# Kernel optimization log

Measured on AMD Instinct MI355X. Metric: run time of the kernel, lower is better.

The kernel has to match this reference:

```python
import jax, jax.numpy as jnp
import numpy as np

B, T, F = 32, 1024, 64
H = 128          # num_lstm_out
KH = 16          # kan_hidden_dim
C1, C2, C3 = 128, 256, 128
NC = 10


def _glorot(key, shape):
    fan_in = shape[0] if len(shape) == 2 else int(np.prod(shape[1:]))
    return (jax.random.normal(key, shape, jnp.float32) / np.sqrt(fan_in)).astype(jnp.float32)


def setup_inputs() -> dict:
    key = jax.random.key(0)
    ks = jax.random.split(key, 24)
    D = F + H
    d = {}
    d['x'] = jax.random.normal(ks[0], (B, T, F), jnp.float32)
    d['eps_z'] = jax.random.normal(ks[1], (B, H), jnp.float32)
    d['eps_cat'] = jax.random.normal(ks[2], (B, H), jnp.float32)
    # KAN-LSTM cell: gates = W2 @ silu(W1 @ [x;h])
    d['kan_w1'] = _glorot(ks[3], (D, KH)); d['kan_b1'] = jnp.zeros((KH,), jnp.float32)
    d['kan_w2'] = _glorot(ks[4], (KH, 4 * H)); d['kan_b2'] = jnp.zeros((4 * H,), jnp.float32)
    # causal convs (OIH layout)
    d['conv1_w'] = _glorot(ks[5], (C1, F, 8)); d['conv1_b'] = jnp.zeros((C1,), jnp.float32)
    d['conv2_w'] = _glorot(ks[6], (C2, C1, 5)); d['conv2_b'] = jnp.zeros((C2,), jnp.float32)
    d['conv3_w'] = _glorot(ks[7], (C3, C2, 3)); d['conv3_b'] = jnp.zeros((C3,), jnp.float32)
    # batchnorm affine params
    d['bn1_g'] = jnp.ones((C1,), jnp.float32); d['bn1_b'] = jnp.zeros((C1,), jnp.float32)
    d['bn2_g'] = jnp.ones((C2,), jnp.float32); d['bn2_b'] = jnp.zeros((C2,), jnp.float32)
    d['bn3_g'] = jnp.ones((C3,), jnp.float32); d['bn3_b'] = jnp.zeros((C3,), jnp.float32)
    # SE layers (reduction=16, no bias)
    d['se1_w1'] = _glorot(ks[8], (C1, C1 // 16)); d['se1_w2'] = _glorot(ks[9], (C1 // 16, C1))
    d['se2_w1'] = _glorot(ks[10], (C2, C2 // 16)); d['se2_w2'] = _glorot(ks[11], (C2 // 16, C2))
    # VIB heads
    d['fc_mu_w'] = _glorot(ks[12], (H, H)); d['fc_mu_b'] = jnp.zeros((H,), jnp.float32)
    d['fc_std_w'] = _glorot(ks[13], (H, H)); d['fc_std_b'] = jnp.zeros((H,), jnp.float32)
    d['fc_mu_cat_w'] = _glorot(ks[14], (2 * H, H)); d['fc_mu_cat_b'] = jnp.zeros((H,), jnp.float32)
    d['fc_std_cat_w'] = _glorot(ks[15], (2 * H, H)); d['fc_std_cat_b'] = jnp.zeros((H,), jnp.float32)
    d['fc_w'] = _glorot(ks[16], (H + C3, NC)); d['fc_b'] = jnp.zeros((NC,), jnp.float32)
    return d


def _kan_lstm(x, w1, b1, w2, b2):
    # x: (B,T,F) -> hidden (B,T,H); sequential recurrence via lax.scan
    xT = jnp.swapaxes(x, 0, 1)  # (T,B,F)
    h0 = jnp.zeros((x.shape[0], H), x.dtype)
    c0 = jnp.zeros((x.shape[0], H), x.dtype)

    def step(carry, xt):
        h, c = carry
        g = jax.nn.silu(jnp.concatenate([xt, h], axis=-1) @ w1 + b1) @ w2 + b2  # (B,4H)
        i_, f_, g_, o_ = jnp.split(g, 4, axis=-1)
        c = jax.nn.sigmoid(f_) * c + jax.nn.sigmoid(i_) * jnp.tanh(g_)
        h = jax.nn.sigmoid(o_) * jnp.tanh(c)
        return (h, c), h

    _, hs = jax.lax.scan(step, (h0, c0), xT)
    return jnp.swapaxes(hs, 0, 1)  # (B,T,H)


def _cluster_hidden(hidden):
    # hidden: (B,T,H). Pairwise cosine sim -> exp kernel -> best 2-block cut.
    Tn = hidden.shape[1]
    last = hidden[:, -1, :]
    hn = hidden / jnp.clip(jnp.linalg.norm(hidden, axis=-1, keepdims=True), 1e-8)
    S = jnp.exp(-5.5 * (1.0 - jnp.einsum('bik,bjk->bij', hn, hn)))  # (B,T,T)
    S = S * (1.0 - jnp.eye(Tn, dtype=S.dtype))  # zero diagonal
    # 2D prefix sums give all block sums in O(T^2) instead of O(T^3)
    P = jnp.cumsum(jnp.cumsum(S, axis=1), axis=2)
    i = jnp.arange(1, Tn)
    TL = P[:, i - 1, i - 1]                 # (B,T-1) sum of [:i,:i]
    full = P[:, -1, -1][:, None]
    TR = P[:, i - 1, -1] - TL               # sum of [:i,i:]
    BL = P[:, -1, i - 1] - TL               # sum of [i:,:i]
    BR = full - TL - TR - BL                # sum of [i:,i:]
    ii = i.astype(S.dtype)
    nn = (Tn - i).astype(S.dtype)
    dist = TL / (ii * ii) + BR / (nn * nn) - (TR + BL) / (ii * nn)
    cuts = jnp.argmax(dist, axis=1) + 1     # (B,)
    mask = (jnp.arange(Tn)[None, :] < cuts[:, None]).astype(hidden.dtype)
    corr = jnp.einsum('bt,bth->bh', mask, hidden) / cuts[:, None].astype(hidden.dtype)
    return last, corr


def _causal_conv(x, w, b):
    k = w.shape[-1]
    xp = jnp.pad(x, ((0, 0), (0, 0), (k - 1, 0)))
    y = jax.lax.conv_general_dilated(xp, w, (1,), 'VALID',
                                     dimension_numbers=('NCH', 'OIH', 'NCH'))
    return y + b[None, :, None]


def _bn(x, g, b, eps=1e-3):
    m = x.mean(axis=(0, 2), keepdims=True)
    v = x.var(axis=(0, 2), keepdims=True)
    return (x - m) / jnp.sqrt(v + eps) * g[None, :, None] + b[None, :, None]


def _se(x, w1, w2):
    y = x.mean(axis=2)                       # (B,C)
    y = jax.nn.sigmoid(jax.nn.relu(y @ w1) @ w2)
    return x * y[:, :, None]


def reference(x, eps_z, eps_cat, kan_w1, kan_b1, kan_w2, kan_b2,
              conv1_w, conv1_b, conv2_w, conv2_b, conv3_w, conv3_b,
              bn1_g, bn1_b, bn2_g, bn2_b, bn3_g, bn3_b,
              se1_w1, se1_w2, se2_w1, se2_w2,
              fc_mu_w, fc_mu_b, fc_std_w, fc_std_b,
              fc_mu_cat_w, fc_mu_cat_b, fc_std_cat_w, fc_std_cat_b,
              fc_w, fc_b):
    # LSTM branch
    hidden = _kan_lstm(x, kan_w1, kan_b1, kan_w2, kan_b2)      # (B,T,H)
    out, corr = _cluster_hidden(hidden)
    mu = corr @ fc_mu_w + fc_mu_b
    std = jax.nn.softplus(corr @ fc_std_w + fc_std_b)
    z = mu + std * eps_z
    xz = jnp.concatenate([out, z], axis=1)                      # (B,2H)
    mu_cat = xz @ fc_mu_cat_w + fc_mu_cat_b
    std_cat = jax.nn.softplus(xz @ fc_std_cat_w + fc_std_cat_b)
    x1 = mu_cat + std_cat * eps_cat   # dropout in eval mode = identity
    # FCN branch
    x2 = jnp.swapaxes(x, 1, 2)                                  # (B,F,T)
    x2 = jax.nn.gelu(_bn(_causal_conv(x2, conv1_w, conv1_b), bn1_g, bn1_b), approximate=False)
    x2 = _se(x2, se1_w1, se1_w2)
    x2 = jax.nn.gelu(_bn(_causal_conv(x2, conv2_w, conv2_b), bn2_g, bn2_b), approximate=False)
    x2 = _se(x2, se2_w1, se2_w2)
    x2 = jax.nn.gelu(_bn(_causal_conv(x2, conv3_w, conv3_b), bn3_g, bn3_b), approximate=False)
    x2 = x2.mean(axis=2)                                        # (B,C3)
    x_all = jnp.concatenate([x1, x2], axis=1)
    logits = x_all @ fc_w + fc_b
    return (jax.nn.log_softmax(logits, axis=1), mu, std, mu_cat, std_cat)
```

## Files before the change

kernel.cpp:

```cpp
#include <hip/hip_runtime.h>
#include <math.h>

#define B_ 32
#define T_ 1024
#define F_ 64
#define H_ 128
#define D_ 192
#define KH_ 16
#define C1_ 128
#define C2_ 256
#define C3_ 128
#define NC_ 10

typedef float v2f __attribute__((ext_vector_type(2)));
typedef float f32x4 __attribute__((ext_vector_type(4)));
typedef __bf16 bfrag __attribute__((ext_vector_type(8)));

__device__ __forceinline__ float sig_(float x){ return 1.f/(1.f+__expf(-x)); }
__device__ __forceinline__ float tanh_(float x){ return 1.f - 2.f/(__expf(2.f*x)+1.f); }
__device__ __forceinline__ float gelu_(float x){ return 0.5f*x*(1.f+erff(x*0.70710678118654752f)); }
__device__ __forceinline__ float softplus_(float x){ return fmaxf(x,0.f) + log1pf(__expf(-fabsf(x))); }

__device__ __forceinline__ unsigned bfpack(float a, float b){
  unsigned ua = __float_as_uint(a), ub = __float_as_uint(b);
  ua = ua + 0x7FFFu + ((ua>>16)&1u);
  ub = ub + 0x7FFFu + ((ub>>16)&1u);
  return (ua>>16) | (ub & 0xFFFF0000u);
}
__device__ __forceinline__ unsigned short bf1(float a){
  unsigned ua = __float_as_uint(a);
  ua = ua + 0x7FFFu + ((ua>>16)&1u);
  return (unsigned short)(ua>>16);
}
__device__ __forceinline__ float bf2f(unsigned short h){
  return __uint_as_float(((unsigned)h)<<16);
}

#define QPERM_XOR1(x) __int_as_float(__builtin_amdgcn_mov_dpp(__float_as_int(x), 0xB1, 0xF, 0xF, true))
#define QPERM_XOR2(x) __int_as_float(__builtin_amdgcn_mov_dpp(__float_as_int(x), 0x4E, 0xF, 0xF, true))

#define LDS_BARRIER() asm volatile("s_waitcnt lgkmcnt(0)\n\ts_barrier" ::: "memory")


__device__ __forceinline__ void ax_body(int blk, char* smemraw,
    const float* __restrict__ x, const float* __restrict__ w1, const float* __restrict__ b1,
    float* __restrict__ axT)
{
  struct AxS { float xs[16][68]; float w1s[64][16]; };
  AxS* sm = (AxS*)smemraw;
  const int bt0 = blk*16;
  const int tid = threadIdx.x;
  for(int i=tid;i<64*16;i+=256){ sm->w1s[i>>4][i&15] = w1[i]; }
  for(int i=tid;i<16*64;i+=256){ const int r=i>>6, d=i&63; sm->xs[r][d] = x[(size_t)(bt0+r)*64 + d]; }
  __syncthreads();
  const int r = tid>>4, j = tid&15;
  float s = b1[j];
  #pragma unroll
  for(int d=0; d<64; d++) s += sm->xs[r][d]*sm->w1s[d][j];
  const int bt = bt0 + r;
  axT[((size_t)(bt>>10)*16 + j)*1024 + (bt&1023)] = s;
}

__device__ __forceinline__ void prepack_body(int blk,
    const float* __restrict__ w1s, const float* __restrict__ w2s, const float* __restrict__ w3s,
    unsigned short* __restrict__ wp1, unsigned short* __restrict__ wp2, unsigned short* __restrict__ wp3)
{
  int e = blk*256 + threadIdx.x;
  if(e >= 65536+163840+98304) return;
  const float* w; unsigned short* wp; int Cout, Cin, Kw;
  if(e < 65536){ w=w1s; wp=wp1; Cout=C1_; Cin=F_;  Kw=8; }
  else if(e < 65536+163840){ e-=65536; w=w2s; wp=wp2; Cout=C2_; Cin=C1_; Kw=5; }
  else { e-=229376; w=w3s; wp=wp3; Cout=C3_; Cin=C2_; Kw=3; }
  const int co = e/(Cin*Kw);
  const int rem = e - co*(Cin*Kw);
  const int ci = rem/Kw, kw = rem - ci*Kw;
  const int off = (((ci>>5)*Kw + kw)*(Cout>>4) + (co>>4))*512 + ((co&15)*4 + ((ci>>3)&3))*8 + (ci&7);
  wp[off] = bf1(w[e]);
}

__device__ __forceinline__ void norm8_body(size_t rowbase,
    const float* __restrict__ hidden,
    unsigned short* __restrict__ hnhi, unsigned short* __restrict__ hnlo)
{
  const size_t row = rowbase + (threadIdx.x>>5);
  const int l = threadIdx.x&31;
  const float* hr = hidden + row*H_;
  float s = 0.f;
  for(int k=l;k<H_;k+=32){ float v=hr[k]; s+=v*v; }
  #pragma unroll
  for(int m=16;m>=1;m>>=1) s += __shfl_xor(s, m, 64);
  const float inv = 1.f/fmaxf(sqrtf(s), 1e-8f);
  const float4 v = *(const float4*)&hr[l*4];
  const float f0=v.x*inv, f1=v.y*inv, f2=v.z*inv, f3=v.w*inv;
  const unsigned short h0=bf1(f0), h1=bf1(f1), h2=bf1(f2), h3=bf1(f3);
  uint2 phi; phi.x = (unsigned)h0 | ((unsigned)h1<<16); phi.y = (unsigned)h2 | ((unsigned)h3<<16);
  *(uint2*)&hnhi[row*H_ + l*4] = phi;
  const unsigned short g0=bf1(f0-bf2f(h0)), g1=bf1(f1-bf2f(h1)), g2=bf1(f2-bf2f(h2)), g3=bf1(f3-bf2f(h3));
  uint2 plo; plo.x = (unsigned)g0 | ((unsigned)g1<<16); plo.y = (unsigned)g2 | ((unsigned)g3<<16);
  *(uint2*)&hnlo[row*H_ + l*4] = plo;
}

__device__ __forceinline__ void chunk_body(int b, int c, char* smemraw,
    const float* __restrict__ hidden, float* __restrict__ chunksum)
{
  float* red = (float*)smemraw;
  const int tid = threadIdx.x, h = tid&127, half = tid>>7;
  const float* hb = hidden + ((size_t)b*T_ + c*64)*H_;
  float s = 0.f;
  for(int t=half; t<64; t+=2) s += hb[(size_t)t*H_ + h];
  if(half==1) red[h] = s;
  __syncthreads();
  if(half==0) chunksum[((size_t)b*16 + c)*H_ + h] = s + red[h];
}

struct SS {
  unsigned short Ahi[64*136];
  unsigned short Alo[64*136];
  unsigned short Bhi[64*136];
  unsigned short Blo[64*136];
  double red[64][17];
};
__device__ __forceinline__ void s_list_body(int b, int f0, int cnt, char* smemraw,
    const unsigned short* __restrict__ hnhi, const unsigned short* __restrict__ hnlo,
    double* __restrict__ rowsum, double* __restrict__ psum)
{
  SS* sm = (SS*)smemraw;
  const int tid = threadIdx.x, l = tid & 63, wv = tid >> 6;
  const int m = l & 15, q = l >> 4;
  const int arow = (wv*16 + m)*136;
  double* red = &sm->red[0][0];
  int curj = -1;

  for(int f=f0; f<f0+cnt; f++){
    int j = (int)((sqrtf(8.f*(float)f + 1.f) - 1.f)*0.5f);
    while((j*(j+1))/2 > f) j--;
    while(((j+1)*(j+2))/2 <= f) j++;
    const int i = f - (j*(j+1))/2;
    const int i0 = i*64, j0 = j*64;

    __syncthreads();
    if(j != curj){
      curj = j;
      const uint4* ghi = (const uint4*)(hnhi + ((size_t)b*T_ + j0)*H_);
      const uint4* glo = (const uint4*)(hnlo + ((size_t)b*T_ + j0)*H_);
      for(int t2=tid; t2<64*16; t2+=256){
        const int r = t2>>4, c8 = t2&15;
        *(uint4*)&sm->Bhi[r*136 + c8*8] = ghi[r*16 + c8];
        *(uint4*)&sm->Blo[r*136 + c8*8] = glo[r*16 + c8];
      }
    }
    {
      const uint4* ghi = (const uint4*)(hnhi + ((size_t)b*T_ + i0)*H_);
      const uint4* glo = (const uint4*)(hnlo + ((size_t)b*T_ + i0)*H_);
      for(int t2=tid; t2<64*16; t2+=256){
        const int r = t2>>4, c8 = t2&15;
        *(uint4*)&sm->Ahi[r*136 + c8*8] = ghi[r*16 + c8];
        *(uint4*)&sm->Alo[r*136 + c8*8] = glo[r*16 + c8];
      }
    }
    __syncthreads();

    f32x4 acc[4];
    #pragma unroll
    for(int nt=0;nt<4;nt++) acc[nt] = (f32x4)(0.f);
    #pragma unroll
    for(int kc=0;kc<4;kc++){
      const bfrag Ah = *(const bfrag*)&sm->Ahi[arow + kc*32 + q*8];
      const bfrag Al = *(const bfrag*)&sm->Alo[arow + kc*32 + q*8];
      #pragma unroll
      for(int nt=0;nt<4;nt++){
        const int brow = (nt*16 + m)*136 + kc*32 + q*8;
        const bfrag Bh = *(const bfrag*)&sm->Bhi[brow];
        const bfrag Bl = *(const bfrag*)&sm->Blo[brow];
        acc[nt] = __builtin_amdgcn_mfma_f32_16x16x32_bf16(Ah, Bh, acc[nt], 0, 0, 0);
        acc[nt] = __builtin_amdgcn_mfma_f32_16x16x32_bf16(Al, Bh, acc[nt], 0, 0, 0);
        acc[nt] = __builtin_amdgcn_mfma_f32_16x16x32_bf16(Ah, Bl, acc[nt], 0, 0, 0);
      }
    }

    if(i0 == j0){
      double rs[4]={0,0,0,0}, ps[4]={0,0,0,0};
      #pragma unroll
      for(int nt=0;nt<4;nt++){
        const int gj = j0 + nt*16 + m;
        #pragma unroll
        for(int r=0;r<4;r++){
          const int gi = i0 + wv*16 + q*4 + r;
          if(gi == gj) continue;
          const float sv = __expf(-5.5f*(1.f - acc[nt][r]));
          rs[r] += (double)sv;
          if(gj < gi) ps[r] += (double)sv;
        }
      }
      #pragma unroll
      for(int r=0;r<4;r++){
        #pragma unroll
        for(int mk=1;mk<16;mk<<=1){
          rs[r] += __shfl_xor(rs[r], mk, 64);
          ps[r] += __shfl_xor(ps[r], mk, 64);
        }
      }
      if(m == 0){
        const size_t gbase = (size_t)b*T_ + i0 + wv*16 + q*4;
        #pragma unroll
        for(int r=0;r<4;r++){
          unsafeAtomicAdd(&rowsum[gbase + r], rs[r]);
          unsafeAtomicAdd(&psum[gbase + r], ps[r]);
        }
      }
    } else {
      double rs[4]={0,0,0,0}, cs[4]={0,0,0,0};
      #pragma unroll
      for(int nt=0;nt<4;nt++){
        double csn = 0.0;
        #pragma unroll
        for(int r=0;r<4;r++){
          const float sv = __expf(-5.5f*(1.f - acc[nt][r]));
          rs[r] += (double)sv;
          csn   += (double)sv;
        }
        cs[nt] = csn;
      }
      #pragma unroll
      for(int r=0;r<4;r++){
        #pragma unroll
        for(int mk=1;mk<16;mk<<=1) rs[r] += __shfl_xor(rs[r], mk, 64);
      }
      if(m == 0){
        const size_t gbase = (size_t)b*T_ + i0 + wv*16 + q*4;
        #pragma unroll
        for(int r=0;r<4;r++) unsafeAtomicAdd(&rowsum[gbase + r], rs[r]);
      }
      #pragma unroll
      for(int nt=0;nt<4;nt++){
        cs[nt] += __shfl_xor(cs[nt], 16, 64);
        cs[nt] += __shfl_xor(cs[nt], 32, 64);
      }
      if(q == 0){
        #pragma unroll
        for(int nt=0;nt<4;nt++) red[wv*64 + nt*16 + m] = cs[nt];
      }
      __syncthreads();
      if(tid < 64){
        const double v = red[tid] + red[64+tid] + red[128+tid] + red[192+tid];
        unsafeAtomicAdd(&rowsum[(size_t)b*T_ + j0 + tid], v);
        unsafeAtomicAdd(&psum[(size_t)b*T_ + j0 + tid], v);
      }
    }
  }
}

struct CS {
  double sr[256]; double sp[256]; double bd[256]; double totR;
  float c2[2][128]; int bidx[256]; int cut;
};
__device__ __forceinline__ void cluster_body(int b, char* smemraw,
    const double* __restrict__ rowsum, const double* __restrict__ psum,
    const float* __restrict__ hidden, const float* __restrict__ chunksum,
    float* __restrict__ corr, int* __restrict__ cuts)
{
  CS* sm = (CS*)smemraw;
  const int tid = threadIdx.x;
  const double* r = rowsum + (size_t)b*T_;
  const double* p = psum + (size_t)b*T_;
  double r4[4], p4[4];
  #pragma unroll
  for(int q=0;q<4;q++){ r4[q]=r[tid*4+q]; p4[q]=p[tid*4+q]; }
  sm->sr[tid]=r4[0]+r4[1]+r4[2]+r4[3];
  sm->sp[tid]=p4[0]+p4[1]+p4[2]+p4[3];
  __syncthreads();
  if(tid==0){
    double ar=0, ap=0;
    for(int i=0;i<256;i++){ double tr=sm->sr[i], tp=sm->sp[i]; sm->sr[i]=ar; sm->sp[i]=ap; ar+=tr; ap+=tp; }
    sm->totR = ar;
  }
  __syncthreads();
  double cr = sm->sr[tid], cp = sm->sp[tid];
  const double full = sm->totR;
  double best = -1e308; int bi = 1;
  #pragma unroll
  for(int q=0;q<4;q++){
    cr += r4[q]; cp += p4[q];
    const int i = 4*tid + q + 1;
    if(i < T_){
      const double TL = 2.0*cp;
      const double TRv = cr - TL;
      const double BR = full - TL - 2.0*TRv;
      const double di = (double)i, dn = (double)(T_-i);
      const double dist = TL/(di*di) + BR/(dn*dn) - (2.0*TRv)/(di*dn);
      if(dist > best){ best=dist; bi=i; }
    }
  }
  sm->bd[tid]=best; sm->bidx[tid]=bi;
  __syncthreads();
  if(tid==0){
    double bb=-1e308; int ii=1;
    for(int q=0;q<256;q++){ if(sm->bd[q]>bb){ bb=sm->bd[q]; ii=sm->bidx[q]; } }
    sm->cut=ii; cuts[b]=ii;
  }
  __syncthreads();
  const int cut = sm->cut;
  const int h = tid&127, half = tid>>7;
  float s=0.f;
  if(half==0){
    const int cf = cut>>6;
    for(int c=0;c<cf;c++) s += chunksum[((size_t)b*16 + c)*H_ + h];
  } else {
    const float* hb = hidden + (size_t)b*T_*H_;
    for(int t=(cut & ~63); t<cut; t++) s += hb[(size_t)t*H_ + h];
  }
  sm->c2[half][h]=s;
  __syncthreads();
  if(tid<128) corr[b*H_+tid] = (sm->c2[0][tid]+sm->c2[1][tid])/(float)cut;
}

__device__ __forceinline__ void head1_body(int b, char* smemraw,
    const float* __restrict__ corr, const float* __restrict__ hidden,
    const float* __restrict__ eps_z, const float* __restrict__ eps_cat,
    const float* __restrict__ mu_w, const float* __restrict__ mu_b,
    const float* __restrict__ std_w, const float* __restrict__ std_b,
    const float* __restrict__ muc_w, const float* __restrict__ muc_b,
    const float* __restrict__ stdc_w, const float* __restrict__ stdc_b,
    float* __restrict__ out_mu, float* __restrict__ out_std,
    float* __restrict__ out_muc, float* __restrict__ out_stdc, float* __restrict__ x1)
{
  struct H1 { float cs[128]; float xz[256]; };
  H1* sm = (H1*)smemraw;
  const int h = threadIdx.x;
  if(h<128){
    sm->cs[h]=corr[b*H_+h];
    sm->xz[h]=hidden[((size_t)b*T_ + (T_-1))*H_ + h];
  }
  __syncthreads();
  if(h<128){
    float m=mu_b[h], sdv=std_b[h];
    for(int k=0;k<H_;k++){ const float cv=sm->cs[k]; m+=cv*mu_w[k*H_+h]; sdv+=cv*std_w[k*H_+h]; }
    const float stdv = softplus_(sdv);
    out_mu[b*H_+h]=m; out_std[b*H_+h]=stdv;
    sm->xz[128+h] = m + stdv*eps_z[b*H_+h];
  }
  __syncthreads();
  if(h<128){
    float mc=muc_b[h], sc=stdc_b[h];
    for(int k=0;k<256;k++){ const float v=sm->xz[k]; mc+=v*muc_w[k*H_+h]; sc+=v*stdc_w[k*H_+h]; }
    const float stdc = softplus_(sc);
    out_muc[b*H_+h]=mc; out_stdc[b*H_+h]=stdc;
    x1[b*H_+h]=mc + stdc*eps_cat[b*H_+h];
  }
}

struct ConvS {
  float sescale[256];
  float seh[16];
  unsigned short xs[72*40];
};
__device__ __forceinline__ void conv_body(int bx, int by, int bz, char* smemraw,
    const float* __restrict__ in, const unsigned short* __restrict__ wp,
    const float* __restrict__ bias,
    const float* __restrict__ se_in, const float* __restrict__ se_w1,
    const float* __restrict__ se_w2, int seR,
    float* __restrict__ y, float* __restrict__ bnacc, int Cin, int Cout, int Kw)
{
  ConvS* sm = (ConvS*)smemraw;
  unsigned short* xs = sm->xs;
  const int b = bz, t0 = bx*64, co0 = by*64;
  const int tid = threadIdx.x, l = tid&63, wv = tid>>6;
  const int q = l>>4, m = l&15;
  const int TW = 64 + Kw - 1;
  const int abase = (wv*16 + m)*40 + q*8;
  const int boff = (m*4 + q)*8;
  const bool use_se = (se_in != nullptr);

  if(use_se){
    float* ms = (float*)xs;
    if(tid<Cin) ms[tid] = se_in[b*Cin+tid] * (1.f/(float)T_);
    __syncthreads();
    if(tid<seR){ float s=0.f; for(int k=0;k<Cin;k++) s += ms[k]*se_w1[k*seR+tid]; sm->seh[tid]=fmaxf(s,0.f); }
    __syncthreads();
    if(tid<Cin){ float s=0.f; for(int k=0;k<seR;k++) s += sm->seh[k]*se_w2[k*Cin+tid]; sm->sescale[tid]=sig_(s); }
  }

  f32x4 acc[4];
  #pragma unroll
  for(int nt=0;nt<4;nt++) acc[nt] = (f32x4)(0.f);

  const int nchunks = Cin >> 5;
  for(int cc=0; cc<nchunks; cc++){
    __syncthreads();
    for(int idx=tid; idx<TW*8; idx+=256){
      const int r = idx>>3, c4 = (idx&7)*4;
      const int tg = t0 - (Kw-1) + r;
      uint2 pk = make_uint2(0u, 0u);
      if(tg >= 0){
        float4 v = *(const float4*)&in[((size_t)b*T_ + tg)*Cin + cc*32 + c4];
        if(use_se){
          const float4 s4 = *(const float4*)&sm->sescale[cc*32 + c4];
          v.x*=s4.x; v.y*=s4.y; v.z*=s4.z; v.w*=s4.w;
        }
        pk.x = bfpack(v.x, v.y); pk.y = bfpack(v.z, v.w);
      }
      *(uint2*)&xs[r*40 + c4] = pk;
    }
    __syncthreads();
    for(int kw=0; kw<Kw; kw++){
      const bfrag Af = *(const bfrag*)&xs[abase + kw*40];
      #pragma unroll
      for(int nt=0; nt<4; nt++){
        const unsigned short* wpp = wp + ((size_t)((cc*Kw + kw)*(Cout>>4) + (by*4 + nt)))*512 + boff;
        const bfrag Bf = *(const bfrag*)wpp;
        acc[nt] = __builtin_amdgcn_mfma_f32_16x16x32_bf16(Af, Bf, acc[nt], 0, 0, 0);
      }
    }
  }
  __syncthreads();
  float* part = (float*)xs;
  const int t_base = t0 + wv*16 + q*4;
  #pragma unroll
  for(int nt=0; nt<4; nt++){
    const int co = co0 + nt*16 + m;
    const float bv = bias[co];
    float s1 = 0.f, s2 = 0.f;
    #pragma unroll
    for(int r=0;r<4;r++){
      const float v = acc[nt][r] + bv;
      y[((size_t)b*T_ + t_base + r)*Cout + co] = v;
      s1 += v; s2 += v*v;
    }
    s1 += __shfl_xor(s1, 16); s1 += __shfl_xor(s1, 32);
    s2 += __shfl_xor(s2, 16); s2 += __shfl_xor(s2, 32);
    if(q==0){ part[(wv*64 + nt*16 + m)*2+0] = s1; part[(wv*64 + nt*16 + m)*2+1] = s2; }
  }
  __syncthreads();
  if(tid < 64){
    float a1=0.f, a2=0.f;
    #pragma unroll
    for(int w2i=0; w2i<4; w2i++){ a1 += part[(w2i*64+tid)*2+0]; a2 += part[(w2i*64+tid)*2+1]; }
    atomicAdd(&bnacc[co0 + tid], a1);
    atomicAdd(&bnacc[Cout + co0 + tid], a2);
  }
}

__device__ __forceinline__ void bn_act_body(int b, int chunk, char* smemraw,
    float* __restrict__ y, const float* __restrict__ bnacc,
    const float* __restrict__ gw, const float* __restrict__ bw,
    float* __restrict__ mean_acc, int C, int write_y)
{
  const int t0 = chunk*128, tid = threadIdx.x;
  const int c = tid & (C-1), part = tid / C, np = 256 / C;
  const float cnt = (float)(B_*T_);
  const float mm = bnacc[c]/cnt;
  const float var = bnacc[C+c]/cnt - mm*mm;
  const float sc = gw[c]/sqrtf(var+1e-3f);
  const float sh = bw[c] - mm*sc;
  float s = 0.f;
  for(int t=t0+part; t<t0+128; t+=np){
    const size_t off = ((size_t)b*T_ + t)*C + c;
    float v = y[off];
    v = gelu_(v*sc + sh);
    if(write_y) y[off] = v;
    s += v;
  }
  float* rs = (float*)smemraw;
  if(np > 1){
    rs[tid]=s;
    __syncthreads();
    if(part==0) s += rs[tid+C];
  }
  if(part==0) atomicAdd(&mean_acc[b*C+c], s);
}

__device__ __forceinline__ void lstm_seg_body(int b, int ts, int nsteps, char* smemraw,
    const float* __restrict__ axT, const float* __restrict__ w1,
    const float* __restrict__ w2, const float* __restrict__ b2,
    float* __restrict__ hidden, float* __restrict__ cstate)
{
  float (*hs)[148] = (float(*)[148])smemraw;
  const int tid = threadIdx.x;
  const int l = tid & 63, wv = tid >> 6;
  const int j = l >> 2, g = l & 3;
  const int hi = wv*64 + l;

  v2f w1hv[16];
  #pragma unroll
  for(int q=0;q<16;q++){
    w1hv[q].x = w1[(64 + g*32 + 2*q)*KH_ + j];
    w1hv[q].y = w1[(64 + g*32 + 2*q + 1)*KH_ + j];
  }
  v2f w2if[16], w2go[16];
  #pragma unroll
  for(int k=0;k<16;k++){
    w2if[k].x = w2[k*512 + hi];       w2if[k].y = w2[k*512 + 128 + hi];
    w2go[k].x = w2[k*512 + 256 + hi]; w2go[k].y = w2[k*512 + 384 + hi];
  }
  v2f bif, bgo;
  bif.x = b2[hi]; bif.y = b2[128+hi]; bgo.x = b2[256+hi]; bgo.y = b2[384+hi];

  const float* axr = axT + ((size_t)b*16 + j)*1024;
  float* hb = hidden + (size_t)b*T_*H_;
  const int hwi = (hi>>5)*36 + (hi&31);
  float c;
  if(ts == 0){
    for(int i=tid;i<2*148;i+=128) ((float*)hs)[i]=0.f;
    c = 0.f;
  } else {
    c = cstate[b*H_ + hi];
    hs[0][hwi] = hb[(size_t)(ts-1)*H_ + hi];
  }
  float4 axA = *(const float4*)&axr[ts];
  float4 axB = *(const float4*)&axr[ts+4];
  __syncthreads();

#define LSTM_STEP(tt, axv, RB) { \
    const float* hsr = hs[RB]; \
    float* hsw = hs[1-(RB)]; \
    v2f ap0=(v2f)(0.f), ap1=(v2f)(0.f), ap2=(v2f)(0.f), ap3=(v2f)(0.f); \
    { const float4 hv = *(const float4*)&hsr[g*36 + 0];  ap0 += ((v2f){hv.x,hv.y})*w1hv[0]  + ((v2f){hv.z,hv.w})*w1hv[1]; } \
    { const float4 hv = *(const float4*)&hsr[g*36 + 4];  ap1 += ((v2f){hv.x,hv.y})*w1hv[2]  + ((v2f){hv.z,hv.w})*w1hv[3]; } \
    { const float4 hv = *(const float4*)&hsr[g*36 + 8];  ap2 += ((v2f){hv.x,hv.y})*w1hv[4]  + ((v2f){hv.z,hv.w})*w1hv[5]; } \
    { const float4 hv = *(const float4*)&hsr[g*36 + 12]; ap3 += ((v2f){hv.x,hv.y})*w1hv[6]  + ((v2f){hv.z,hv.w})*w1hv[7]; } \
    { const float4 hv = *(const float4*)&hsr[g*36 + 16]; ap0 += ((v2f){hv.x,hv.y})*w1hv[8]  + ((v2f){hv.z,hv.w})*w1hv[9]; } \
    { const float4 hv = *(const float4*)&hsr[g*36 + 20]; ap1 += ((v2f){hv.x,hv.y})*w1hv[10] + ((v2f){hv.z,hv.w})*w1hv[11]; } \
    { const float4 hv = *(const float4*)&hsr[g*36 + 24]; ap2 += ((v2f){hv.x,hv.y})*w1hv[12] + ((v2f){hv.z,hv.w})*w1hv[13]; } \
    { const float4 hv = *(const float4*)&hsr[g*36 + 28]; ap3 += ((v2f){hv.x,hv.y})*w1hv[14] + ((v2f){hv.z,hv.w})*w1hv[15]; } \
    const v2f apt = (ap0+ap1)+(ap2+ap3); \
    float a = apt.x + apt.y; \
    a += QPERM_XOR1(a); \
    a += QPERM_XOR2(a); \
    a += (axv); \
    const float g1 = a * sig_(a); \
    v2f aIF = bif, aGO = bgo; \
    _Pragma("unroll") \
    for(int k=0;k<16;k++){ \
      const float gk = __int_as_float(__builtin_amdgcn_readlane(__float_as_int(g1), 4*k)); \
      v2f gk2; gk2.x=gk; gk2.y=gk; \
      aIF += gk2 * w2if[k]; \
      aGO += gk2 * w2go[k]; \
    } \
    const float si = sig_(aIF.x); \
    const float sf = sig_(aIF.y); \
    const float tg = tanh_(aGO.x); \
    const float so = sig_(aGO.y); \
    c = sf*c + si*tg; \
    const float h = so * tanh_(c); \
    hsw[hwi] = h; \
    hb[(size_t)(tt)*H_ + hi] = h; \
    LDS_BARRIER(); \
  }

  const int te = ts + nsteps;
  for(int t0=ts;t0<te;t0+=4){
    const int tl = (t0+8 < 1020) ? (t0+8) : 1020;
    const float4 axC = *(const float4*)&axr[tl];
    LSTM_STEP(t0+0, axA.x, 0)
    LSTM_STEP(t0+1, axA.y, 1)
    LSTM_STEP(t0+2, axA.z, 0)
    LSTM_STEP(t0+3, axA.w, 1)
    axA = axB; axB = axC;
  }
#undef LSTM_STEP
  if(te < T_) cstate[b*H_ + hi] = c;
}


__global__ __launch_bounds__(256) void mega0_kernel(
    const float* c1w, const float* c2w, const float* c3w,
    unsigned short* wp1, unsigned short* wp2, unsigned short* wp3,
    const float* x, const float* kw1, const float* kb1, float* axT)
{
  __shared__ __align__(16) char sm[16*68*4 + 64*16*4];
  const int bid = blockIdx.x;
  if(bid < 256) prepack_body(bid, c1w, c2w, c3w, wp1, wp2, wp3);
  else ax_body(bid-256, sm, x, kw1, kb1, axT);
}

__global__ __launch_bounds__(256) void seg_kernel(
    int ts, int nsteps, int phase, int nphase, int nxtra,
    int nr0, int nnorm, int c0, int nchunk,
    const float* axT, const float* kw1, const float* kw2, const float* kb2,
    float* hidden, float* cstate,
    const float* x, const unsigned short* wp1, const float* c1b, float* y1, float* bn1,
    const float* g1w, const float* b1w, float* se1_in,
    const unsigned short* wp2, const float* c2b, const float* s1w1, const float* s1w2,
    float* y2, float* bn2,
    const float* g2w, const float* b2w, float* se2_in,
    const unsigned short* wp3, const float* c3b, const float* s2w1, const float* s2w2,
    float* y3, float* bn3,
    const float* c1w, const float* c2w, const float* c3w,
    unsigned short* wp1o, unsigned short* wp2o, unsigned short* wp3o,
    unsigned short* hnhi, unsigned short* hnlo, float* chunksum)
{
  __shared__ __align__(16) char sm[sizeof(ConvS)];
  const int bid = blockIdx.x;
  if(bid < 32){
    if(nsteps == 0) return;
    if(threadIdx.x >= 128){
      const int nb = nsteps + 1;
      #pragma nounroll
      for(int i=0;i<nb;i++){ asm volatile("s_barrier" ::: "memory"); }
      return;
    }
    __builtin_amdgcn_s_setprio(1);
    lstm_seg_body(bid, ts, nsteps, sm, axT, kw1, kw2, kb2, hidden, cstate);
    return;
  }
  int cb = bid - 32;
  if(cb < nphase){
    switch(phase){
      case 0:
        conv_body(cb&15, (cb>>4)&1, cb>>5, sm, x, wp1, c1b,
                  nullptr, nullptr, nullptr, 0, y1, bn1, F_, C1_, 8);
        break;
      case 1:
        bn_act_body(cb>>3, cb&7, sm, y1, bn1, g1w, b1w, se1_in, C1_, 1);
        break;
      case 2:
        conv_body(cb&15, (cb>>4)&3, cb>>6, sm, y1, wp2, c2b,
                  se1_in, s1w1, s1w2, C1_/16, y2, bn2, C1_, C2_, 5);
        break;
      case 3:
        bn_act_body(cb>>3, cb&7, sm, y2, bn2, g2w, b2w, se2_in, C2_, 1);
        break;
      default:
        conv_body(cb&15, (cb>>4)&1, cb>>5, sm, y2, wp3, c3b,
                  se2_in, s2w1, s2w2, C2_/16, y3, bn3, C2_, C3_, 3);
        break;
    }
    return;
  }
  cb -= nphase;
  if(cb < nxtra){ prepack_body(256 + cb, c1w, c2w, c3w, wp1o, wp2o, wp3o); return; }
  cb -= nxtra;
  if(cb < nnorm){
    const int b = cb & 31, tb = cb >> 5;
    norm8_body((size_t)b*T_ + nr0 + tb*8, hidden, hnhi, hnlo);
    return;
  }
  cb -= nnorm;
  if(cb < nchunk){
    const int b = cb & 31;
    chunk_body(b, c0 + (cb>>5), sm, hidden, chunksum);
  }
}

__global__ __launch_bounds__(256) void segS_kernel(
    int ts, int nsteps, int nbn3,
    int nr0, int nnorm, int c0, int nchunk,
    int smode, int sringlo, int nstile,
    const float* axT, const float* kw1, const float* kw2, const float* kb2,
    float* hidden, float* cstate,
    float* y3, const float* bn3, const float* g3w, const float* b3w, float* x2,
    unsigned short* hnhi, unsigned short* hnlo, float* chunksum,
    double* rowsum, double* psum)
{
  __shared__ __align__(16) char sm[sizeof(SS)];
  const int bid = blockIdx.x;
  if(bid < 32){
    if(nsteps == 0) return;
    if(threadIdx.x >= 128){
      const int nb = nsteps + 1;
      #pragma nounroll
      for(int i=0;i<nb;i++){ asm volatile("s_barrier" ::: "memory"); }
      return;
    }
    __builtin_amdgcn_s_setprio(1);
    lstm_seg_body(bid, ts, nsteps, sm, axT, kw1, kw2, kb2, hidden, cstate);
    return;
  }
  int cb = bid - 32;
  if(cb < nbn3){
    bn_act_body(cb>>3, cb&7, sm, y3, bn3, g3w, b3w, x2, C3_, 0);
    return;
  }
  cb -= nbn3;
  if(cb < nnorm){
    const int b = cb & 31, tb = cb >> 5;
    norm8_body((size_t)b*T_ + nr0 + tb*8, hidden, hnhi, hnlo);
    return;
  }
  cb -= nnorm;
  if(cb < nchunk){
    const int b = cb & 31;
    chunk_body(b, c0 + (cb>>5), sm, hidden, chunksum);
    return;
  }
  cb -= nchunk;
  if(cb < nstile){
    const int b = cb & 31, k = cb >> 5;
    int f0, cnt;
    if(smode == 1){
      const int m = sringlo + k;
      f0 = (m*(m+1))/2; cnt = m + 1;
    } else {
      f0 = 55 + ((k<9) ? 7*k : 63 + 6*(k-9));
      cnt = (k<9) ? 7 : 6;
    }
    s_list_body(b, f0, cnt, sm, hnhi, hnlo, rowsum, psum);
  }
}

__global__ __launch_bounds__(256) void tail_kernel(
    const double* rowsum, const double* psum, const float* hidden,
    const float* chunksum, float* corr, int* cuts,
    const float* eps_z, const float* eps_cat,
    const float* mu_w, const float* mu_b, const float* std_w, const float* std_b,
    const float* muc_w, const float* muc_b, const float* stdc_w, const float* stdc_b,
    float* out_mu, float* out_std, float* out_muc, float* out_stdc, float* x1,
    const float* x2, const float* fcw, const float* fcb, float* outls)
{
  __shared__ __align__(16) char sm[sizeof(CS)];
  const int b = blockIdx.x, tid = threadIdx.x;
  cluster_body(b, sm, rowsum, psum, hidden, chunksum, corr, cuts);
  __syncthreads();
  head1_body(b, sm, corr, hidden, eps_z, eps_cat, mu_w, mu_b, std_w, std_b,
             muc_w, muc_b, stdc_w, stdc_b, out_mu, out_std, out_muc, out_stdc, x1);
  __syncthreads();
  struct H2 { float xa[256]; float lg[NC_]; };
  H2* s2 = (H2*)sm;
  s2->xa[tid] = (tid<128) ? x1[b*128+tid] : x2[b*128+(tid-128)]*(1.f/(float)T_);
  __syncthreads();
  if(tid<NC_){
    float s = fcb[tid];
    for(int k=0;k<256;k++) s += s2->xa[k]*fcw[k*NC_+tid];
    s2->lg[tid]=s;
  }
  __syncthreads();
  if(tid==0){
    float mx=s2->lg[0];
    for(int q=1;q<NC_;q++) mx=fmaxf(mx,s2->lg[q]);
    float se=0;
    for(int q=0;q<NC_;q++) se += __expf(s2->lg[q]-mx);
    const float lse = logf(se)+mx;
    for(int q=0;q<NC_;q++) outls[b*NC_+q] = s2->lg[q]-lse;
  }
}

extern "C" void kernel_launch(void* const* d_in, const int* in_sizes, int n_in,
                              void* d_out, int out_size, void* d_ws, size_t ws_size,
                              hipStream_t stream) {
  (void)in_sizes; (void)n_in; (void)out_size; (void)ws_size;
  const float* x        = (const float*)d_in[0];
  const float* eps_z    = (const float*)d_in[1];
  const float* eps_cat  = (const float*)d_in[2];
  const float* kan_w1   = (const float*)d_in[3];
  const float* kan_b1   = (const float*)d_in[4];
  const float* kan_w2   = (const float*)d_in[5];
  const float* kan_b2   = (const float*)d_in[6];
  const float* conv1_w  = (const float*)d_in[7];
  const float* conv1_b  = (const float*)d_in[8];
  const float* conv2_w  = (const float*)d_in[9];
  const float* conv2_b  = (const float*)d_in[10];
  const float* conv3_w  = (const float*)d_in[11];
  const float* conv3_b  = (const float*)d_in[12];
  const float* bn1_g    = (const float*)d_in[13];
  const float* bn1_b    = (const float*)d_in[14];
  const float* bn2_g    = (const float*)d_in[15];
  const float* bn2_b    = (const float*)d_in[16];
  const float* bn3_g    = (const float*)d_in[17];
  const float* bn3_b    = (const float*)d_in[18];
  const float* se1_w1   = (const float*)d_in[19];
  const float* se1_w2   = (const float*)d_in[20];
  const float* se2_w1   = (const float*)d_in[21];
  const float* se2_w2   = (const float*)d_in[22];
  const float* fc_mu_w  = (const float*)d_in[23];
  const float* fc_mu_b  = (const float*)d_in[24];
  const float* fc_std_w = (const float*)d_in[25];
  const float* fc_std_b = (const float*)d_in[26];
  const float* fc_muc_w = (const float*)d_in[27];
  const float* fc_muc_b = (const float*)d_in[28];
  const float* fc_stdc_w= (const float*)d_in[29];
  const float* fc_stdc_b= (const float*)d_in[30];
  const float* fc_w     = (const float*)d_in[31];
  const float* fc_b     = (const float*)d_in[32];

  float* out = (float*)d_out;
  float* out_ls   = out;
  float* out_mu   = out + 320;
  float* out_std  = out + 320 + 4096;
  float* out_muc  = out + 320 + 2*4096;
  float* out_stdc = out + 320 + 3*4096;

  float* ws = (float*)d_ws;
  const size_t SZ_HID = (size_t)B_*T_*H_;
  const size_t SZ_Y1  = (size_t)B_*T_*C1_;
  const size_t SZ_Y2  = (size_t)B_*T_*C2_;
  float*  hidden = ws;
  float*  y1     = hidden + SZ_HID;
  float*  y2     = y1 + SZ_Y1;
  double* rowsum = (double*)(y2 + SZ_Y2);
  double* psum   = rowsum + (size_t)B_*T_;
  float*  corr   = (float*)(psum + (size_t)B_*T_);
  float*  x1     = corr + (size_t)B_*H_;
  float*  bnbuf  = x1 + (size_t)B_*H_;
  float*  bn1    = bnbuf;
  float*  bn2    = bnbuf + 2*C1_;
  float*  bn3    = bnbuf + 2*C1_ + 2*C2_;
  float*  se1_in = bnbuf + 1024;
  float*  se2_in = se1_in + (size_t)B_*C1_;
  float*  x2     = se2_in + (size_t)B_*C2_;
  int*    cuts   = (int*)(x2 + (size_t)B_*C3_);
  float*  cstate = (float*)(cuts + B_);
  float*  chunksum = cstate + (size_t)B_*H_;
  float*  axbuf  = chunksum + (size_t)B_*16*H_;
  unsigned short* wp1 = (unsigned short*)(axbuf + (size_t)B_*16*T_);
  unsigned short* wp2 = wp1 + (size_t)C1_*F_*8;
  unsigned short* wp3 = wp2 + (size_t)C2_*C1_*5;
  unsigned short* hnhi = wp3 + (size_t)C3_*C2_*3;
  unsigned short* hnlo = hnhi + (size_t)B_*T_*H_;
  float*  y3     = y1;

  hipMemsetAsync(bnbuf, 0, (size_t)(1024 + B_*C1_ + B_*C2_ + B_*C3_)*sizeof(float), stream);
  hipMemsetAsync(rowsum, 0, (size_t)2*B_*T_*sizeof(double), stream);

  mega0_kernel<<<2304, 256, 0, stream>>>(conv1_w, conv2_w, conv3_w, wp1, wp2, wp3,
                                         x, kan_w1, kan_b1, axbuf);

  #define SEG_ARGS axbuf, kan_w1, kan_w2, kan_b2, hidden, cstate, \
      x, wp1, conv1_b, y1, bn1, bn1_g, bn1_b, se1_in, \
      wp2, conv2_b, se1_w1, se1_w2, y2, bn2, bn2_g, bn2_b, se2_in, \
      wp3, conv3_b, se2_w1, se2_w2, y3, bn3, \
      conv1_w, conv2_w, conv3_w, wp1, wp2, wp3, \
      hnhi, hnlo, chunksum
  seg_kernel<<<32+1024+1024, 256, 0, stream>>>(  0,144, 0,1024,1024,   0,   0,  0,  0, SEG_ARGS);
  seg_kernel<<<32+256+576,   256, 0, stream>>>(144, 64, 1, 256,   0,   0, 576,  0,  0, SEG_ARGS);
  seg_kernel<<<32+2048+256+96,256,0, stream>>>(208,384, 2,2048,   0, 144, 256,  0, 96, SEG_ARGS);
  seg_kernel<<<32+256+1536+192,256,0,stream>>>(592, 64, 3, 256,   0, 208,1536,  3,192, SEG_ARGS);
  seg_kernel<<<32+1024+256+32,256,0, stream>>>(656,240, 4,1024,   0, 592, 256,  9, 32, SEG_ARGS);
  #undef SEG_ARGS

  #define SEGS_ARGS axbuf, kan_w1, kan_w2, kan_b2, hidden, cstate, \
      y3, bn3, bn3_g, bn3_b, x2, hnhi, hnlo, chunksum, rowsum, psum
  segS_kernel<<<32+256+960+128+320, 256, 0, stream>>>(
      896, 128, 256, 656, 960, 10, 128, 1, 0, 320, SEGS_ARGS);
  {
    #define SEG_ARGS axbuf, kan_w1, kan_w2, kan_b2, hidden, cstate, \
        x, wp1, conv1_b, y1, bn1, bn1_g, bn1_b, se1_in, \
        wp2, conv2_b, se1_w1, se1_w2, y2, bn2, bn2_g, bn2_b, se2_in, \
        wp3, conv3_b, se2_w1, se2_w2, y3, bn3, \
        conv1_w, conv2_w, conv3_w, wp1, wp2, wp3, \
        hnhi, hnlo, chunksum
    seg_kernel<<<32+512+64, 256, 0, stream>>>(0, 0, -1, 0, 0, 896, 512, 14, 64, SEG_ARGS);
    #undef SEG_ARGS
  }
  segS_kernel<<<32+384, 256, 0, stream>>>(
      0, 0, 0, 0, 0, 0, 0, 2, 0, 384, SEGS_ARGS);
  #undef SEGS_ARGS

  tail_kernel<<<B_, 256, 0, stream>>>(rowsum, psum, hidden, chunksum, corr, cuts,
      eps_z, eps_cat,
      fc_mu_w, fc_mu_b, fc_std_w, fc_std_b, fc_muc_w, fc_muc_b, fc_stdc_w, fc_stdc_b,
      out_mu, out_std, out_muc, out_stdc, x1,
      x2, fc_w, fc_b, out_ls);
}
```

Before: 726.1 us.

## Defer most input projection work into segment kernels and rebalance LSTM segments

Result: slower. 790.9 us (+8.9%).

```diff
diff --git a/kernel.cpp b/kernel.cpp
--- a/kernel.cpp
+++ b/kernel.cpp
@@ -570,13 +570,16 @@
   __shared__ __align__(16) char sm[16*68*4 + 64*16*4];
   const int bid = blockIdx.x;
   if(bid < 256) prepack_body(bid, c1w, c2w, c3w, wp1, wp2, wp3);
-  else ax_body(bid-256, sm, x, kw1, kb1, axT);
+  else {
+    const int idx = bid - 256;
+    ax_body((idx>>4)*64 + (idx&15), sm, x, kw1, kb1, axT);
+  }
 }
 
 __global__ __launch_bounds__(256) void seg_kernel(
-    int ts, int nsteps, int phase, int nphase, int nxtra,
+    int ts, int nsteps, int phase, int nphase, int nxtra, int nax,
     int nr0, int nnorm, int c0, int nchunk,
-    const float* axT, const float* kw1, const float* kw2, const float* kb2,
+    float* axT, const float* kw1, const float* kb1, const float* kw2, const float* kb2,
     float* hidden, float* cstate,
     const float* x, const unsigned short* wp1, const float* c1b, float* y1, float* bn1,
     const float* g1w, const float* b1w, float* se1_in,
@@ -589,7 +592,7 @@
     unsigned short* wp1o, unsigned short* wp2o, unsigned short* wp3o,
     unsigned short* hnhi, unsigned short* hnlo, float* chunksum)
 {
-  __shared__ __align__(16) char sm[sizeof(ConvS)];
+  __shared__ __align__(16) char sm[16*68*4 + 64*16*4];
   const int bid = blockIdx.x;
   if(bid < 32){
     if(nsteps == 0) return;
@@ -630,6 +633,12 @@
   cb -= nphase;
   if(cb < nxtra){ prepack_body(256 + cb, c1w, c2w, c3w, wp1o, wp2o, wp3o); return; }
   cb -= nxtra;
+  if(cb < nax){
+    const int bb = cb/48, tb2 = cb - bb*48;
+    ax_body(bb*64 + 16 + tb2, sm, x, kw1, kb1, axT);
+    return;
+  }
+  cb -= nax;
   if(cb < nnorm){
     const int b = cb & 31, tb = cb >> 5;
     norm8_body((size_t)b*T_ + nr0 + tb*8, hidden, hnhi, hnlo);
@@ -645,7 +654,7 @@
 __global__ __launch_bounds__(256) void segS_kernel(
     int ts, int nsteps, int nbn3,
     int nr0, int nnorm, int c0, int nchunk,
-    int smode, int sringlo, int nstile,
+    int smode, int sp0, int sbsz, int stot, int nstile,
     const float* axT, const float* kw1, const float* kw2, const float* kb2,
     float* hidden, float* cstate,
     float* y3, const float* bn3, const float* g3w, const float* b3w, float* x2,
@@ -688,11 +697,12 @@
     const int b = cb & 31, k = cb >> 5;
     int f0, cnt;
     if(smode == 1){
-      const int m = sringlo + k;
+      const int m = sp0 + k;
       f0 = (m*(m+1))/2; cnt = m + 1;
     } else {
-      f0 = 55 + ((k<9) ? 7*k : 63 + 6*(k-9));
-      cnt = (k<9) ? 7 : 6;
+      f0 = sp0 + k*sbsz;
+      cnt = sp0 + stot - f0;
+      if(cnt > sbsz) cnt = sbsz;
     }
     s_list_body(b, f0, cnt, sm, hnhi, hnlo, rowsum, psum);
   }
@@ -811,38 +821,35 @@
   hipMemsetAsync(bnbuf, 0, (size_t)(1024 + B_*C1_ + B_*C2_ + B_*C3_)*sizeof(float), stream);
   hipMemsetAsync(rowsum, 0, (size_t)2*B_*T_*sizeof(double), stream);
 
-  mega0_kernel<<<2304, 256, 0, stream>>>(conv1_w, conv2_w, conv3_w, wp1, wp2, wp3,
-                                         x, kan_w1, kan_b1, axbuf);
-
-  #define SEG_ARGS axbuf, kan_w1, kan_w2, kan_b2, hidden, cstate, \
+  mega0_kernel<<<768, 256, 0, stream>>>(conv1_w, conv2_w, conv3_w, wp1, wp2, wp3,
+                                        x, kan_w1, kan_b1, axbuf);
+
+  #define SEG_ARGS axbuf, kan_w1, kan_b1, kan_w2, kan_b2, hidden, cstate, \
       x, wp1, conv1_b, y1, bn1, bn1_g, bn1_b, se1_in, \
       wp2, conv2_b, se1_w1, se1_w2, y2, bn2, bn2_g, bn2_b, se2_in, \
       wp3, conv3_b, se2_w1, se2_w2, y3, bn3, \
       conv1_w, conv2_w, conv3_w, wp1, wp2, wp3, \
       hnhi, hnlo, chunksum
-  seg_kernel<<<32+1024+1024, 256, 0, stream>>>(  0,144, 0,1024,1024,   0,   0,  0,  0, SEG_ARGS);
-  seg_kernel<<<32+256+576,   256, 0, stream>>>(144, 64, 1, 256,   0,   0, 576,  0,  0, SEG_ARGS);
-  seg_kernel<<<32+2048+256+96,256,0, stream>>>(208,384, 2,2048,   0, 144, 256,  0, 96, SEG_ARGS);
-  seg_kernel<<<32+256+1536+192,256,0,stream>>>(592, 64, 3, 256,   0, 208,1536,  3,192, SEG_ARGS);
-  seg_kernel<<<32+1024+256+32,256,0, stream>>>(656,240, 4,1024,   0, 592, 256,  9, 32, SEG_ARGS);
+  seg_kernel<<<32+1024+1024+1536, 256, 0, stream>>>(
+        0,208, 0,1024, 1024,1536,   0,   0,  0,  0, SEG_ARGS);
+  seg_kernel<<<32+256, 256, 0, stream>>>(
+        0,  0, 1, 256,    0,   0,   0,   0,  0,  0, SEG_ARGS);
+  seg_kernel<<<32+2048+832+96, 256, 0, stream>>>(
+      208,448, 2,2048,    0,   0,   0, 832,  0, 96, SEG_ARGS);
+  seg_kernel<<<32+256, 256, 0, stream>>>(
+        0,  0, 3, 256,    0,   0,   0,   0,  0,  0, SEG_ARGS);
+  seg_kernel<<<32+1024+1792+224, 256, 0, stream>>>(
+      656,240, 4,1024,    0,   0, 208,1792,  3,224, SEG_ARGS);
   #undef SEG_ARGS
 
   #define SEGS_ARGS axbuf, kan_w1, kan_w2, kan_b2, hidden, cstate, \
       y3, bn3, bn3_g, bn3_b, x2, hnhi, hnlo, chunksum, rowsum, psum
   segS_kernel<<<32+256+960+128+320, 256, 0, stream>>>(
-      896, 128, 256, 656, 960, 10, 128, 1, 0, 320, SEGS_ARGS);
-  {
-    #define SEG_ARGS axbuf, kan_w1, kan_w2, kan_b2, hidden, cstate, \
-        x, wp1, conv1_b, y1, bn1, bn1_g, bn1_b, se1_in, \
-        wp2, conv2_b, se1_w1, se1_w2, y2, bn2, bn2_g, bn2_b, se2_in, \
-        wp3, conv3_b, se2_w1, se2_w2, y3, bn3, \
-        conv1_w, conv2_w, conv3_w, wp1, wp2, wp3, \
-        hnhi, hnlo, chunksum
-    seg_kernel<<<32+512+64, 256, 0, stream>>>(0, 0, -1, 0, 0, 896, 512, 14, 64, SEG_ARGS);
-    #undef SEG_ARGS
-  }
-  segS_kernel<<<32+384, 256, 0, stream>>>(
-      0, 0, 0, 0, 0, 0, 0, 2, 0, 384, SEGS_ARGS);
+      896, 128, 256, 656, 960, 10, 128, 1, 0, 0, 0, 320, SEGS_ARGS);
+  segS_kernel<<<32+512+64+256, 256, 0, stream>>>(
+      0, 0, 0, 896, 512, 14, 64, 2, 55, 7, 50, 256, SEGS_ARGS);
+  segS_kernel<<<32+160, 256, 0, stream>>>(
+      0, 0, 0, 0, 0, 0, 0, 2, 105, 7, 31, 160, SEGS_ARGS);
   #undef SEGS_ARGS
 
   tail_kernel<<<B_, 256, 0, stream>>>(rowsum, psum, hidden, chunksum, corr, cuts,
```
